# Optimization experiments

Measured on AMD Instinct MI355X. Metric: run time of the kernel, lower is better.

The kernel has to match this reference:

```python
import jax, jax.numpy as jnp
import numpy as np

BETA = 10.0


def _read_buffer(alpha, B, s_b, pop):
    # alpha: [b], B: [b,S,H], s_b: [b,S]. Closed form of the saturating
    # sequential read: cumsum after i steps = min(prefix_sum(s_b)_i, alpha),
    # so weight_i = min(P_i, alpha) - min(P_{i-1}, alpha).
    P = jnp.cumsum(s_b, axis=1)
    Pc = jnp.minimum(P, alpha[:, None])
    w = Pc - jnp.concatenate([jnp.zeros_like(Pc[:, :1]), Pc[:, :-1]], axis=1)
    vec = jnp.einsum('bs,bsh->bh', w, B)
    return vec, (s_b - w if pop else s_b)


def _read_stack(alpha, V, s, pop):
    # V: [M,b,H], s: [M,b]; smaller index = closer to stack top (unused slots
    # above the top have s==0 and contribute nothing).
    P = jnp.cumsum(s, axis=0)                 # [M,b]
    a = alpha[None, :]
    Pc1 = jnp.minimum(P, a)                   # saturate at alpha (first read)
    Pc2 = jnp.minimum(P, 1.0 + a)             # saturate at 1+alpha (both reads)
    z = jnp.zeros_like(P[:1])
    w1 = Pc1 - jnp.concatenate([z, Pc1[:-1]], axis=0)
    wt = Pc2 - jnp.concatenate([z, Pc2[:-1]], axis=0)
    w2 = wt - w1
    v1 = jnp.einsum('mb,mbh->bh', w1, V)
    v2 = jnp.einsum('mb,mbh->bh', w2, V)
    return v1, v2, (s - wt if pop else s)


def _forward(x, emb_table, lstm_wih, lstm_whh, lstm_bih, lstm_bhh,
             alpha_w, alpha_b, tree_left_w, tree_left_b, tree_right_w,
             tree_right_b, l0_w, l0_b, l1_w, l1_b, l2_w, l2_b):
    b, S = x.shape
    H = emb_table.shape[1]
    time = 2 * S
    M = 1 + 2 * time                          # max stack depth
    B = emb_table[x]                          # [b,S,H]
    s_b0 = (x > 0).astype(jnp.float32)
    V0 = jnp.zeros((M, b, H), jnp.float32)    # initial sentinel at M-1 (zeros)
    s0 = jnp.zeros((M, b), jnp.float32)
    h0 = jnp.zeros((b, H), jnp.float32)
    c0 = jnp.zeros((b, H), jnp.float32)
    ones_b = jnp.ones((b,), jnp.float32)

    def step(carry, t):
        s_b, V, s, h, c = carry
        n = 1 + 2 * t                         # current number of stack items
        x_b, _ = _read_buffer(ones_b, B, s_b, False)
        x1, x2, _ = _read_stack(ones_b, V, s, False)
        xt = jnp.concatenate([x_b, x1, x2], axis=1)
        # LSTMCell (torch gate order i,f,g,o)
        g = xt @ lstm_wih.T + lstm_bih + h @ lstm_whh.T + lstm_bhh
        gi, gf, gg, go = jnp.split(g, 4, axis=1)
        c = jax.nn.sigmoid(gf) * c + jax.nn.sigmoid(gi) * jnp.tanh(gg)
        h = jax.nn.sigmoid(go) * jnp.tanh(c)
        alphas = jax.nn.softmax(BETA * (h @ alpha_w.T + alpha_b), axis=1)
        a_r, a_s = alphas[:, 0], alphas[:, 1]
        # reduce: pop ~2 items, treeLSTM, push result with strength alpha_r
        r1, r2, s = _read_stack(a_r, V, s, True)
        tg = r1 @ tree_left_w.T + tree_left_b + r2 @ tree_right_w.T + tree_right_b
        ta, ti, tf1, tf2, to = jnp.split(tg, 5, axis=1)
        ct = jnp.tanh(ta) * jax.nn.sigmoid(ti) + jax.nn.sigmoid(tf1) * r1 + jax.nn.sigmoid(tf2) * r2
        ht = jax.nn.sigmoid(to) * jnp.tanh(ct)
        idx = M - (n + 1)
        V = V.at[idx].set(ht)
        s = s.at[idx].set(a_r)
        # shift: pop from buffer with strength alpha_s, push onto stack
        buf, s_b = _read_buffer(a_s, B, s_b, True)
        idx2 = M - (n + 2)
        V = V.at[idx2].set(buf)
        s = s.at[idx2].set(a_s)
        return (s_b, V, s, h, c), None

    carry, _ = jax.lax.scan(jax.checkpoint(step), (s_b0, V0, s0, h0, c0),
                            jnp.arange(time))
    s_b, V, s, h, c = carry
    x1, _, _ = _read_stack(ones_b, V, s, False)
    # MLP head
    y = jax.nn.relu(x1 @ l0_w.T + l0_b)
    y = jax.nn.relu(y @ l1_w.T + l1_b)
    return y @ l2_w.T + l2_b


def setup_inputs() -> dict:
    key = jax.random.key(0)
    ks = jax.random.split(key, 12)
    b, S, H, V, MLP, C = 64, 48, 256, 50257, 1024, 3
    sc = 0.05
    return {
        'x': jax.random.randint(ks[0], (b, S), 0, V, dtype=jnp.int32).astype(jnp.int64),
        'emb_table': jax.random.normal(ks[1], (V, H), jnp.float32) * sc,
        'lstm_wih': jax.random.normal(ks[2], (4 * H, 3 * H), jnp.float32) * sc,
        'lstm_whh': jax.random.normal(ks[3], (4 * H, H), jnp.float32) * sc,
        'lstm_bih': jnp.zeros((4 * H,), jnp.float32),
        'lstm_bhh': jnp.zeros((4 * H,), jnp.float32),
        'alpha_w': jax.random.normal(ks[4], (2, H), jnp.float32) * sc,
        'alpha_b': jnp.zeros((2,), jnp.float32),
        'tree_left_w': jax.random.normal(ks[5], (5 * H, H), jnp.float32) * sc,
        'tree_left_b': jnp.zeros((5 * H,), jnp.float32),
        'tree_right_w': jax.random.normal(ks[6], (5 * H, H), jnp.float32) * sc,
        'tree_right_b': jnp.zeros((5 * H,), jnp.float32),
        'l0_w': jax.random.normal(ks[7], (MLP, H), jnp.float32) * sc,
        'l0_b': jnp.zeros((MLP,), jnp.float32),
        'l1_w': jax.random.normal(ks[8], (MLP, MLP), jnp.float32) * sc,
        'l1_b': jnp.zeros((MLP,), jnp.float32),
        'l2_w': jax.random.normal(ks[9], (C, MLP), jnp.float32) * sc,
        'l2_b': jnp.zeros((C,), jnp.float32),
    }


def reference(x, emb_table, lstm_wih, lstm_whh, lstm_bih, lstm_bhh, alpha_w,
              alpha_b, tree_left_w, tree_left_b, tree_right_w, tree_right_b,
              l0_w, l0_b, l1_w, l1_b, l2_w, l2_b):
    return _forward(x, emb_table, lstm_wih, lstm_whh, lstm_bih, lstm_bhh,
                    alpha_w, alpha_b, tree_left_w, tree_left_b, tree_right_w,
                    tree_right_b, l0_w, l0_b, l1_w, l1_b, l2_w, l2_b)
```

## Files before the change

### kernel.cpp

```cpp
#include <hip/hip_runtime.h>
#include <math.h>

#define NBLK 1024
#define NTHR 256

typedef float vf4 __attribute__((ext_vector_type(4)));

namespace spinn {

constexpr int Ss = 48, Hh = 256, TT = 96, Mm = 193, H3 = 768, MLPD = 1024;

__device__ __forceinline__ float sigf(float x) { return 1.0f / (1.0f + expf(-x)); }

#define FMA4(acc, a, b)                         \
    {                                           \
        acc.x = fmaf((a).x, (b).x, acc.x);      \
        acc.y = fmaf((a).y, (b).y, acc.y);      \
        acc.z = fmaf((a).z, (b).z, acc.z);      \
        acc.w = fmaf((a).w, (b).w, acc.w);      \
    }

__device__ __forceinline__ void st_co(float* p, float v) {
    asm volatile("global_store_dword %0, %1, off sc0 sc1" :: "v"(p), "v"(v) : "memory");
}
__device__ __forceinline__ void ld_co_v4_1(const vf4* p0, vf4& r0) {
    asm volatile("global_load_dwordx4 %0, %1, off sc0 sc1\n\t"
                 "s_waitcnt vmcnt(0)"
                 : "=&v"(r0) : "v"(p0) : "memory");
}
__device__ __forceinline__ void ld_co_f1x4(const float* p0, const float* p1, const float* p2,
                                           const float* p3, float& r0, float& r1, float& r2, float& r3) {
    asm volatile("global_load_dword %0, %4, off sc0 sc1\n\t"
                 "global_load_dword %1, %5, off sc0 sc1\n\t"
                 "global_load_dword %2, %6, off sc0 sc1\n\t"
                 "global_load_dword %3, %7, off sc0 sc1\n\t"
                 "s_waitcnt vmcnt(0)"
                 : "=&v"(r0), "=&v"(r1), "=&v"(r2), "=&v"(r3)
                 : "v"(p0), "v"(p1), "v"(p2), "v"(p3) : "memory");
}
__device__ __forceinline__ unsigned ld_co_u32(const unsigned* p) {
    unsigned r;
    asm volatile("global_load_dword %0, %1, off sc0 sc1\n\t"
                 "s_waitcnt vmcnt(0)"
                 : "=&v"(r) : "v"(p) : "memory");
    return r;
}

__device__ __forceinline__ void gbar(unsigned* cnt, unsigned tgt) {
    asm volatile("s_waitcnt vmcnt(0)" ::: "memory");
    __syncthreads();
    if (threadIdx.x == 0) {
        unsigned one = 1u;
        asm volatile("global_atomic_add %0, %1, off" :: "v"(cnt), "v"(one) : "memory");
        while (ld_co_u32(cnt) < tgt) __builtin_amdgcn_s_sleep(1);
    }
    __syncthreads();
}

__device__ __forceinline__ float wave_iscan(float v, int lane) {
    #pragma unroll
    for (int off = 1; off < 64; off <<= 1) {
        float u = __shfl_up(v, off, 64);
        if (lane >= off) v += u;
    }
    return v;
}
__device__ __forceinline__ float wred64(float v) {
    #pragma unroll
    for (int off = 1; off < 64; off <<= 1) v += __shfl_xor(v, off, 64);
    return v;
}
__device__ __forceinline__ float wred_ms(float v) {
    v += __shfl_xor(v, 16, 64);
    v += __shfl_xor(v, 32, 64);
    return v;
}

}

using namespace spinn;

__global__ void __launch_bounds__(NTHR, 4) spinn_kernel(
    const int* __restrict__ x, const float* __restrict__ emb,
    const float* __restrict__ wih, const float* __restrict__ whh,
    const float* __restrict__ bih, const float* __restrict__ bhh,
    const float* __restrict__ aw, const float* __restrict__ ab,
    const float* __restrict__ tlw, const float* __restrict__ tlb,
    const float* __restrict__ trw, const float* __restrict__ trb,
    const float* __restrict__ l0w, const float* __restrict__ l0b,
    const float* __restrict__ l1w, const float* __restrict__ l1b,
    const float* __restrict__ l2w, const float* __restrict__ l2b,
    float* __restrict__ out, float* __restrict__ wsf, unsigned* __restrict__ bar)
{
    const int tid  = threadIdx.x;
    const int bid  = blockIdx.x;
    const int e    = bid >> 4;
    const int q    = bid & 15;
    const int db   = q * 16;
    const int wave = tid >> 6;
    const int lane = tid & 63;
    const int ms   = lane >> 4;
    const int dl   = lane & 15;

    unsigned* cnt = bar + e * 32;
    unsigned barnum = 0;

    float* XTg = wsf;
    float* Hbg = XTg + 64 * H3;
    float* R1g = Hbg + 64 * Hh;
    float* R2g = R1g + 64 * Hh;
    float* Y0g = R2g + 64 * Hh;
    float* Y1g = Y0g + 64 * MLPD;

    __shared__ float s_V[196 * 16];
    __shared__ float s_B[Ss * 16];
    __shared__ float s_xt[H3];
    __shared__ float s_h[256];
    __shared__ float s_c[16];
    __shared__ float s_g[64];
    __shared__ float s_tg[80];
    __shared__ float s_r1[256], s_r2[256];
    __shared__ float s_s[208];
    __shared__ float sw1[208], sw2[208];
    __shared__ float pw1[208], pw2[208];
    __shared__ float s_sb[Ss], s_wb[Ss], s_wbe[Ss];
    __shared__ float s_bias[64];
    __shared__ float s_tbias[80];

    float* s_y = s_V;

    {
        if (tid < 192) {
            int s = tid >> 2, j = tid & 3;
            int tok = x[e * Ss + s];
            ((vf4*)s_B)[tid] = ((const vf4*)emb)[(size_t)tok * 64 + q * 4 + j];
        }
        if (tid < Ss) s_sb[tid] = (x[e * Ss + tid] > 0) ? 1.0f : 0.0f;
        for (int i = tid; i < 208; i += NTHR) s_s[i] = 0.0f;
        if (tid < 256) s_h[tid] = 0.0f;
        if (tid < 16) s_c[tid] = 0.0f;
        if (tid < 64) {
            int row = (tid >> 4) * Hh + db + (tid & 15);
            s_bias[tid] = bih[row] + bhh[row];
        }
        if (tid < 80) {
            int row = (tid >> 4) * Hh + db + (tid & 15);
            s_tbias[tid] = tlb[row] + trb[row];
        }
        for (int i = tid; i < 196 * 16; i += NTHR) s_V[i] = 0.0f;
        __syncthreads();
        if (wave == 0) {
            float sbv = (lane < Ss) ? s_sb[lane] : 0.0f;
            float P = wave_iscan(sbv, lane);
            float wbe = fminf(P, 1.0f) - fminf(P - sbv, 1.0f);
            if (lane < Ss) s_wbe[lane] = wbe;
            float axb = 0.0f;
            #pragma unroll
            for (int j = 0; j < 12; j++) {
                int s = ms * 12 + j;
                axb = fmaf(s_wbe[s], s_B[s * 16 + dl], axb);
            }
            axb = wred_ms(axb);
            if (lane < 16) {
                float* xte = XTg + (size_t)e * H3;
                st_co(xte + db + dl, axb);
                st_co(xte + 256 + db + dl, 0.0f);
                st_co(xte + 512 + db + dl, 0.0f);
            }
        }
    }
    gbar(cnt, ++barnum * 16);

    for (int t = 0; t < TT; t++) {
        const int idx  = 191 - 2 * t;
        const int idx2 = idx - 1;

        {
            if (tid < 192) {
                vf4 v;
                ld_co_v4_1((const vf4*)XTg + (size_t)e * 192 + tid, v);
                ((vf4*)s_xt)[tid] = v;
            }
            __syncthreads();
            vf4 xr0 = ((const vf4*)s_xt)[lane];
            vf4 xr1 = ((const vf4*)s_xt)[64 + lane];
            vf4 xr2 = ((const vf4*)s_xt)[128 + lane];
            vf4 hr  = ((const vf4*)s_h)[lane];
            #pragma unroll 2
            for (int p = 0; p < 16; p++) {
                int r = wave * 16 + p;
                int row = (wave << 8) + db + p;
                const vf4* w  = (const vf4*)wih + (size_t)row * 192;
                const vf4* wh = (const vf4*)whh + (size_t)row * 64;
                vf4 w0 = w[lane], w1 = w[64 + lane], w2 = w[128 + lane], w3 = wh[lane];
                vf4 acc = {0.f, 0.f, 0.f, 0.f};
                FMA4(acc, w0, xr0); FMA4(acc, w1, xr1);
                FMA4(acc, w2, xr2); FMA4(acc, w3, hr);
                float sv = wred64(acc.x + acc.y + acc.z + acc.w);
                if (lane == 0) s_g[r] = sv + s_bias[r];
            }
            __syncthreads();
            if (tid < 16) {
                float gi = s_g[tid], gf = s_g[16 + tid], gg = s_g[32 + tid], go = s_g[48 + tid];
                float cv = sigf(gf) * s_c[tid] + sigf(gi) * tanhf(gg);
                s_c[tid] = cv;
                float hv = sigf(go) * tanhf(cv);
                st_co(Hbg + (size_t)e * Hh + db + tid, hv);
            }
        }
        gbar(cnt, ++barnum * 16);

        if (wave < 2) {
            float h0, h1, h2, h3;
            const float* hb = Hbg + (size_t)e * Hh + lane;
            ld_co_f1x4(hb, hb + 64, hb + 128, hb + 192, h0, h1, h2, h3);
            if (wave == 0) {
                s_h[lane] = h0;       s_h[64 + lane] = h1;
                s_h[128 + lane] = h2; s_h[192 + lane] = h3;
            }
            float lg0 = h0 * aw[lane] + h1 * aw[64 + lane] + h2 * aw[128 + lane] + h3 * aw[192 + lane];
            float lg1 = h0 * aw[256 + lane] + h1 * aw[320 + lane] + h2 * aw[384 + lane] + h3 * aw[448 + lane];
            lg0 = wred64(lg0) + ab[0];
            lg1 = wred64(lg1) + ab[1];
            float a_r = 1.0f / (1.0f + expf(10.0f * (lg1 - lg0)));
            float a_s = 1.0f / (1.0f + expf(10.0f * (lg0 - lg1)));

            if (wave == 0) {
                int m0 = lane * 4;
                float v0 = (m0     < Mm) ? s_s[m0]     : 0.0f;
                float v1 = (m0 + 1 < Mm) ? s_s[m0 + 1] : 0.0f;
                float v2 = (m0 + 2 < Mm) ? s_s[m0 + 2] : 0.0f;
                float v3 = (m0 + 3 < Mm) ? s_s[m0 + 3] : 0.0f;
                float c1 = v0 + v1, c2 = c1 + v2, c3 = c2 + v3;
                float inc = c3;
                #pragma unroll
                for (int off = 1; off < 64; off <<= 1) {
                    float u = __shfl_up(inc, off, 64);
                    if (lane >= off) inc += u;
                }
                float ex = inc - c3;
                float Pv[4]  = {ex + v0, ex + c1, ex + c2, ex + c3};
                float Pp[4]  = {ex, ex + v0, ex + c1, ex + c2};
                float vv_[4] = {v0, v1, v2, v3};
                float sn[4];
                #pragma unroll
                for (int i = 0; i < 4; i++) {
                    int m = m0 + i;
                    float w1 = fminf(Pv[i], a_r) - fminf(Pp[i], a_r);
                    float wt = fminf(Pv[i], 1.0f + a_r) - fminf(Pp[i], 1.0f + a_r);
                    float s2 = vv_[i] - wt;
                    if (m == idx)  s2 = a_r;
                    if (m == idx2) s2 = a_s;
                    sn[i] = s2;
                    if (m < Mm) {
                        sw1[m] = w1;
                        sw2[m] = wt - w1;
                        s_s[m] = s2;
                    } else if (m < 208) {
                        sw1[m] = 0.0f; sw2[m] = 0.0f;
                    }
                }
                float d1 = sn[0] + sn[1], d2 = d1 + sn[2], d3 = d2 + sn[3];
                float inc2 = d3;
                #pragma unroll
                for (int off = 1; off < 64; off <<= 1) {
                    float u = __shfl_up(inc2, off, 64);
                    if (lane >= off) inc2 += u;
                }
                float ex2 = inc2 - d3;
                float Qv[4] = {ex2 + sn[0], ex2 + d1, ex2 + d2, ex2 + d3};
                float Qp[4] = {ex2, ex2 + sn[0], ex2 + d1, ex2 + d2};
                #pragma unroll
                for (int i = 0; i < 4; i++) {
                    int m = m0 + i;
                    if (m < Mm) {
                        float w1e = fminf(Qv[i], 1.0f) - fminf(Qp[i], 1.0f);
                        pw1[m] = w1e;
                        pw2[m] = (fminf(Qv[i], 2.0f) - fminf(Qp[i], 2.0f)) - w1e;
                    } else if (m < 208) {
                        pw1[m] = 0.0f; pw2[m] = 0.0f;
                    }
                }
                float a1 = 0.0f, a2 = 0.0f;
                #pragma unroll 7
                for (int k = 0; k < 49; k++) {
                    int m = ms * 49 + k;
                    float vv = s_V[m * 16 + dl];
                    a1 = fmaf(sw1[m], vv, a1);
                    a2 = fmaf(sw2[m], vv, a2);
                }
                a1 = wred_ms(a1); a2 = wred_ms(a2);
                if (lane < 16) {
                    st_co(R1g + (size_t)e * Hh + db + dl, a1);
                    st_co(R2g + (size_t)e * Hh + db + dl, a2);
                }
            } else {
                float sbv = (lane < Ss) ? s_sb[lane] : 0.0f;
                float Pb = wave_iscan(sbv, lane);
                float wb = fminf(Pb, a_s) - fminf(Pb - sbv, a_s);
                float sbn = sbv - wb;
                float Pb2 = wave_iscan(sbn, lane);
                float wbe = fminf(Pb2, 1.0f) - fminf(Pb2 - sbn, 1.0f);
                if (lane < Ss) { s_sb[lane] = sbn; s_wb[lane] = wb; s_wbe[lane] = wbe; }
                float abf = 0.0f, axb = 0.0f;
                #pragma unroll
                for (int j = 0; j < 12; j++) {
                    int s = ms * 12 + j;
                    float be = s_B[s * 16 + dl];
                    abf = fmaf(s_wb[s], be, abf);
                    axb = fmaf(s_wbe[s], be, axb);
                }
                abf = wred_ms(abf); axb = wred_ms(axb);
                if (lane < 16) {
                    s_V[idx2 * 16 + dl] = abf;
                    st_co(XTg + (size_t)e * H3 + db + dl, axb);
                }
            }
        }
        gbar(cnt, ++barnum * 16);

        {
            if (tid < 64) {
                vf4 v; ld_co_v4_1((const vf4*)R1g + (size_t)e * 64 + tid, v);
                ((vf4*)s_r1)[tid] = v;
            } else if (tid < 128) {
                vf4 v; ld_co_v4_1((const vf4*)R2g + (size_t)e * 64 + (tid - 64), v);
                ((vf4*)s_r2)[tid - 64] = v;
            }
            __syncthreads();
            vf4 r1v = ((const vf4*)s_r1)[lane];
            vf4 r2v = ((const vf4*)s_r2)[lane];
            #pragma unroll 2
            for (int p = 0; p < 20; p++) {
                int r = wave * 20 + p;
                int row = ((r >> 4) << 8) + db + (r & 15);
                const vf4* wl = (const vf4*)tlw + (size_t)row * 64;
                const vf4* wr = (const vf4*)trw + (size_t)row * 64;
                vf4 u = wl[lane], v = wr[lane];
                vf4 acc = {0.f, 0.f, 0.f, 0.f};
                FMA4(acc, u, r1v); FMA4(acc, v, r2v);
                float sv = wred64(acc.x + acc.y + acc.z + acc.w);
                if (lane == 0) s_tg[r] = sv + s_tbias[r];
            }
            __syncthreads();
            if (tid < 16) {
                float ta  = s_tg[tid];
                float ti  = s_tg[16 + tid];
                float tf1 = s_tg[32 + tid];
                float tf2 = s_tg[48 + tid];
                float to  = s_tg[64 + tid];
                float r1d = s_r1[db + tid];
                float r2d = s_r2[db + tid];
                float ct = tanhf(ta) * sigf(ti) + sigf(tf1) * r1d + sigf(tf2) * r2d;
                s_V[idx * 16 + tid] = sigf(to) * tanhf(ct);
            }
            __syncthreads();
            if (wave == 0) {
                float x1 = 0.0f, x2 = 0.0f;
                #pragma unroll 7
                for (int k = 0; k < 49; k++) {
                    int m = ms * 49 + k;
                    float vv = s_V[m * 16 + dl];
                    x1 = fmaf(pw1[m], vv, x1);
                    x2 = fmaf(pw2[m], vv, x2);
                }
                x1 = wred_ms(x1); x2 = wred_ms(x2);
                if (lane < 16) {
                    st_co(XTg + (size_t)e * H3 + 256 + db + dl, x1);
                    st_co(XTg + (size_t)e * H3 + 512 + db + dl, x2);
                }
            }
        }
        gbar(cnt, ++barnum * 16);
    }

    {
        if (tid < 64) {
            vf4 v; ld_co_v4_1((const vf4*)XTg + (size_t)e * 192 + 64 + tid, v);
            ((vf4*)s_y)[tid] = v;
        }
        __syncthreads();
        vf4 xin = ((const vf4*)s_y)[lane];
        #pragma unroll 2
        for (int p = 0; p < 16; p++) {
            int row = q * 64 + wave * 16 + p;
            const vf4* w = (const vf4*)l0w + (size_t)row * 64;
            vf4 wv = w[lane];
            vf4 acc = {0.f, 0.f, 0.f, 0.f};
            FMA4(acc, wv, xin);
            float sv = wred64(acc.x + acc.y + acc.z + acc.w);
            if (lane == 0) st_co(Y0g + (size_t)e * MLPD + row, fmaxf(sv + l0b[row], 0.0f));
        }
    }
    gbar(cnt, ++barnum * 16);
    {
        {
            vf4 v; ld_co_v4_1((const vf4*)Y0g + (size_t)e * 256 + tid, v);
            ((vf4*)s_y)[tid] = v;
        }
        __syncthreads();
        vf4 y0 = ((const vf4*)s_y)[lane],       y1 = ((const vf4*)s_y)[64 + lane];
        vf4 y2 = ((const vf4*)s_y)[128 + lane], y3 = ((const vf4*)s_y)[192 + lane];
        #pragma unroll 2
        for (int p = 0; p < 16; p++) {
            int row = q * 64 + wave * 16 + p;
            const vf4* w = (const vf4*)l1w + (size_t)row * 256;
            vf4 w0 = w[lane], w1 = w[64 + lane], w2 = w[128 + lane], w3 = w[192 + lane];
            vf4 acc = {0.f, 0.f, 0.f, 0.f};
            FMA4(acc, w0, y0); FMA4(acc, w1, y1); FMA4(acc, w2, y2); FMA4(acc, w3, y3);
            float sv = wred64(acc.x + acc.y + acc.z + acc.w);
            if (lane == 0) st_co(Y1g + (size_t)e * MLPD + row, fmaxf(sv + l1b[row], 0.0f));
        }
    }
    gbar(cnt, ++barnum * 16);
    if (q == 0) {
        {
            vf4 v; ld_co_v4_1((const vf4*)Y1g + (size_t)e * 256 + tid, v);
            ((vf4*)s_y)[tid] = v;
        }
        __syncthreads();
        if (tid < 192) {
            int r = tid >> 6;
            const vf4* w = (const vf4*)l2w + (size_t)r * 256;
            vf4 acc = {0.f, 0.f, 0.f, 0.f};
            #pragma unroll
            for (int j = 0; j < 4; j++) {
                vf4 wv = w[lane + j * 64], yv = ((const vf4*)s_y)[lane + j * 64];
                FMA4(acc, wv, yv);
            }
            float sv = wred64(acc.x + acc.y + acc.z + acc.w);
            if (lane == 0) out[e * 3 + r] = sv + l2b[r];
        }
    }
}

extern "C" void kernel_launch(void* const* d_in, const int* in_sizes, int n_in,
                              void* d_out, int out_size, void* d_ws, size_t ws_size,
                              hipStream_t stream) {
    (void)in_sizes; (void)n_in; (void)out_size; (void)ws_size;
    (void)hipMemsetAsync(d_ws, 0, 8192, stream);

    const int*   x_   = (const int*)d_in[0];
    const float* emb  = (const float*)d_in[1];
    const float* wih  = (const float*)d_in[2];
    const float* whh  = (const float*)d_in[3];
    const float* bih  = (const float*)d_in[4];
    const float* bhh  = (const float*)d_in[5];
    const float* aw   = (const float*)d_in[6];
    const float* ab   = (const float*)d_in[7];
    const float* tlw  = (const float*)d_in[8];
    const float* tlb  = (const float*)d_in[9];
    const float* trw  = (const float*)d_in[10];
    const float* trb  = (const float*)d_in[11];
    const float* l0w  = (const float*)d_in[12];
    const float* l0b  = (const float*)d_in[13];
    const float* l1w  = (const float*)d_in[14];
    const float* l1b  = (const float*)d_in[15];
    const float* l2w  = (const float*)d_in[16];
    const float* l2b  = (const float*)d_in[17];

    float* wsf = (float*)((char*)d_ws + 8192);
    unsigned* bar = (unsigned*)d_ws;

    spinn_kernel<<<dim3(NBLK), dim3(NTHR), 0, stream>>>(
        x_, emb, wih, whh, bih, bhh, aw, ab, tlw, tlb, trw, trb,
        l0w, l0b, l1w, l1b, l2w, l2b, (float*)d_out, wsf, bar);
}
```

Baseline: 3.185 ms.

## Distribute alpha logits, precompute stack-read partials, and shorten the per-step critical path

Each block now computes its own partial of the alpha-gate logits right after the LSTM cell and publishes it to a small global array. The next phase reduces those 32 partials instead of every block reloading the full hidden state and doing a 256-wide dot. The x1/x2 stack reads are computed ahead of time by a spare wave, excluding the slot that has not been written yet. The final step then adds only the new slot's contribution, which removes a block barrier and a 49-step loop from the tree phase's serial tail. The hidden state is also loaded by otherwise idle threads during the LSTM phase, and several loop unroll factors are raised. The cost is an extra scratch buffer and more coherent global stores per step.

```diff
diff --git a/kernel.cpp b/kernel.cpp
--- a/kernel.cpp
+++ b/kernel.cpp
@@ -28,15 +28,12 @@
                  "s_waitcnt vmcnt(0)"
                  : "=&v"(r0) : "v"(p0) : "memory");
 }
-__device__ __forceinline__ void ld_co_f1x4(const float* p0, const float* p1, const float* p2,
-                                           const float* p3, float& r0, float& r1, float& r2, float& r3) {
-    asm volatile("global_load_dword %0, %4, off sc0 sc1\n\t"
-                 "global_load_dword %1, %5, off sc0 sc1\n\t"
-                 "global_load_dword %2, %6, off sc0 sc1\n\t"
-                 "global_load_dword %3, %7, off sc0 sc1\n\t"
+__device__ __forceinline__ float ld_co_f1(const float* p) {
+    float r;
+    asm volatile("global_load_dword %0, %1, off sc0 sc1\n\t"
                  "s_waitcnt vmcnt(0)"
-                 : "=&v"(r0), "=&v"(r1), "=&v"(r2), "=&v"(r3)
-                 : "v"(p0), "v"(p1), "v"(p2), "v"(p3) : "memory");
+                 : "=&v"(r) : "v"(p) : "memory");
+    return r;
 }
 __device__ __forceinline__ unsigned ld_co_u32(const unsigned* p) {
     unsigned r;
@@ -111,6 +108,7 @@
     float* R2g = R1g + 64 * Hh;
     float* Y0g = R2g + 64 * Hh;
     float* Y1g = Y0g + 64 * MLPD;
+    float* AP  = Y1g + 64 * MLPD;
 
     __shared__ float s_V[196 * 16];
     __shared__ float s_B[Ss * 16];
@@ -124,6 +122,8 @@
     __shared__ float sw1[208], sw2[208];
     __shared__ float pw1[208], pw2[208];
     __shared__ float s_sb[Ss], s_wb[Ss], s_wbe[Ss];
+    __shared__ float s_wx[2];
+    __shared__ float s_xp1[16], s_xp2[16];
     __shared__ float s_bias[64];
     __shared__ float s_tbias[80];
 
@@ -137,8 +137,10 @@
         }
         if (tid < Ss) s_sb[tid] = (x[e * Ss + tid] > 0) ? 1.0f : 0.0f;
         for (int i = tid; i < 208; i += NTHR) s_s[i] = 0.0f;
-        if (tid < 256) s_h[tid] = 0.0f;
-        if (tid < 16) s_c[tid] = 0.0f;
+        if (tid < 16) {
+            s_c[tid] = 0.0f;
+            st_co(Hbg + (size_t)e * Hh + db + tid, 0.0f);
+        }
         if (tid < 64) {
             int row = (tid >> 4) * Hh + db + (tid & 15);
             s_bias[tid] = bih[row] + bhh[row];
@@ -180,13 +182,17 @@
                 vf4 v;
                 ld_co_v4_1((const vf4*)XTg + (size_t)e * 192 + tid, v);
                 ((vf4*)s_xt)[tid] = v;
+            } else {
+                vf4 v;
+                ld_co_v4_1((const vf4*)Hbg + (size_t)e * 64 + (tid - 192), v);
+                ((vf4*)s_h)[tid - 192] = v;
             }
             __syncthreads();
             vf4 xr0 = ((const vf4*)s_xt)[lane];
             vf4 xr1 = ((const vf4*)s_xt)[64 + lane];
             vf4 xr2 = ((const vf4*)s_xt)[128 + lane];
             vf4 hr  = ((const vf4*)s_h)[lane];
-            #pragma unroll 2
+            #pragma unroll 4
             for (int p = 0; p < 16; p++) {
                 int r = wave * 16 + p;
                 int row = (wave << 8) + db + p;
@@ -206,25 +212,35 @@
                 s_c[tid] = cv;
                 float hv = sigf(go) * tanhf(cv);
                 st_co(Hbg + (size_t)e * Hh + db + tid, hv);
+                float p0 = hv * aw[db + tid];
+                float p1 = hv * aw[256 + db + tid];
+                #pragma unroll
+                for (int off = 1; off < 16; off <<= 1) {
+                    p0 += __shfl_xor(p0, off, 64);
+                    p1 += __shfl_xor(p1, off, 64);
+                }
+                if (tid == 0) {
+                    st_co(AP + e * 32 + q * 2, p0);
+                    st_co(AP + e * 32 + q * 2 + 1, p1);
+                }
             }
         }
         gbar(cnt, ++barnum * 16);
 
-        if (wave < 2) {
-            float h0, h1, h2, h3;
-            const float* hb = Hbg + (size_t)e * Hh + lane;
-            ld_co_f1x4(hb, hb + 64, hb + 128, hb + 192, h0, h1, h2, h3);
-            if (wave == 0) {
-                s_h[lane] = h0;       s_h[64 + lane] = h1;
-                s_h[128 + lane] = h2; s_h[192 + lane] = h3;
-            }
-            float lg0 = h0 * aw[lane] + h1 * aw[64 + lane] + h2 * aw[128 + lane] + h3 * aw[192 + lane];
-            float lg1 = h0 * aw[256 + lane] + h1 * aw[320 + lane] + h2 * aw[384 + lane] + h3 * aw[448 + lane];
-            lg0 = wred64(lg0) + ab[0];
-            lg1 = wred64(lg1) + ab[1];
-            float a_r = 1.0f / (1.0f + expf(10.0f * (lg1 - lg0)));
-            float a_s = 1.0f / (1.0f + expf(10.0f * (lg0 - lg1)));
-
+        {
+            float a_r = 0.0f, a_s = 0.0f;
+            if (wave < 2) {
+                float apv = 0.0f;
+                if (lane < 32) apv = ld_co_f1(AP + e * 32 + lane);
+                apv += __shfl_xor(apv, 2, 64);
+                apv += __shfl_xor(apv, 4, 64);
+                apv += __shfl_xor(apv, 8, 64);
+                apv += __shfl_xor(apv, 16, 64);
+                float lg0 = __shfl(apv, 0, 64) + ab[0];
+                float lg1 = __shfl(apv, 1, 64) + ab[1];
+                a_r = 1.0f / (1.0f + expf(10.0f * (lg1 - lg0)));
+                a_s = 1.0f / (1.0f + expf(10.0f * (lg0 - lg1)));
+            }
             if (wave == 0) {
                 int m0 = lane * 4;
                 float v0 = (m0     < Mm) ? s_s[m0]     : 0.0f;
@@ -275,26 +291,15 @@
                     int m = m0 + i;
                     if (m < Mm) {
                         float w1e = fminf(Qv[i], 1.0f) - fminf(Qp[i], 1.0f);
+                        float w2e = (fminf(Qv[i], 2.0f) - fminf(Qp[i], 2.0f)) - w1e;
                         pw1[m] = w1e;
-                        pw2[m] = (fminf(Qv[i], 2.0f) - fminf(Qp[i], 2.0f)) - w1e;
+                        pw2[m] = w2e;
+                        if (m == idx) { s_wx[0] = w1e; s_wx[1] = w2e; }
                     } else if (m < 208) {
                         pw1[m] = 0.0f; pw2[m] = 0.0f;
                     }
                 }
-                float a1 = 0.0f, a2 = 0.0f;
-                #pragma unroll 7
-                for (int k = 0; k < 49; k++) {
-                    int m = ms * 49 + k;
-                    float vv = s_V[m * 16 + dl];
-                    a1 = fmaf(sw1[m], vv, a1);
-                    a2 = fmaf(sw2[m], vv, a2);
-                }
-                a1 = wred_ms(a1); a2 = wred_ms(a2);
-                if (lane < 16) {
-                    st_co(R1g + (size_t)e * Hh + db + dl, a1);
-                    st_co(R2g + (size_t)e * Hh + db + dl, a2);
-                }
-            } else {
+            } else if (wave == 1) {
                 float sbv = (lane < Ss) ? s_sb[lane] : 0.0f;
                 float Pb = wave_iscan(sbv, lane);
                 float wb = fminf(Pb, a_s) - fminf(Pb - sbv, a_s);
@@ -316,6 +321,33 @@
                     st_co(XTg + (size_t)e * H3 + db + dl, axb);
                 }
             }
+            __syncthreads();
+            if (wave == 0) {
+                float a1 = 0.0f, a2 = 0.0f;
+                #pragma unroll 7
+                for (int k = 0; k < 49; k++) {
+                    int m = ms * 49 + k;
+                    float vv = s_V[m * 16 + dl];
+                    a1 = fmaf(sw1[m], vv, a1);
+                    a2 = fmaf(sw2[m], vv, a2);
+                }
+                a1 = wred_ms(a1); a2 = wred_ms(a2);
+                if (lane < 16) {
+                    st_co(R1g + (size_t)e * Hh + db + dl, a1);
+                    st_co(R2g + (size_t)e * Hh + db + dl, a2);
+                }
+            } else if (wave == 2) {
+                float x1 = 0.0f, x2 = 0.0f;
+                #pragma unroll 7
+                for (int k = 0; k < 49; k++) {
+                    int m = ms * 49 + k;
+                    float vv = s_V[m * 16 + dl];
+                    x1 = fmaf(pw1[m], vv, x1);
+                    x2 = fmaf(pw2[m], vv, x2);
+                }
+                x1 = wred_ms(x1); x2 = wred_ms(x2);
+                if (lane < 16) { s_xp1[dl] = x1; s_xp2[dl] = x2; }
+            }
         }
         gbar(cnt, ++barnum * 16);
 
@@ -330,7 +362,7 @@
             __syncthreads();
             vf4 r1v = ((const vf4*)s_r1)[lane];
             vf4 r2v = ((const vf4*)s_r2)[lane];
-            #pragma unroll 2
+            #pragma unroll 4
             for (int p = 0; p < 20; p++) {
                 int r = wave * 20 + p;
                 int row = ((r >> 4) << 8) + db + (r & 15);
@@ -352,23 +384,12 @@
                 float r1d = s_r1[db + tid];
                 float r2d = s_r2[db + tid];
                 float ct = tanhf(ta) * sigf(ti) + sigf(tf1) * r1d + sigf(tf2) * r2d;
-                s_V[idx * 16 + tid] = sigf(to) * tanhf(ct);
-            }
-            __syncthreads();
-            if (wave == 0) {
-                float x1 = 0.0f, x2 = 0.0f;
-                #pragma unroll 7
-                for (int k = 0; k < 49; k++) {
-                    int m = ms * 49 + k;
-                    float vv = s_V[m * 16 + dl];
-                    x1 = fmaf(pw1[m], vv, x1);
-                    x2 = fmaf(pw2[m], vv, x2);
-                }
-                x1 = wred_ms(x1); x2 = wred_ms(x2);
-                if (lane < 16) {
-                    st_co(XTg + (size_t)e * H3 + 256 + db + dl, x1);
-                    st_co(XTg + (size_t)e * H3 + 512 + db + dl, x2);
-                }
+                float ht = sigf(to) * tanhf(ct);
+                s_V[idx * 16 + tid] = ht;
+                float x1f = fmaf(s_wx[0], ht, s_xp1[tid]);
+                float x2f = fmaf(s_wx[1], ht, s_xp2[tid]);
+                st_co(XTg + (size_t)e * H3 + 256 + db + tid, x1f);
+                st_co(XTg + (size_t)e * H3 + 512 + db + tid, x2f);
             }
         }
         gbar(cnt, ++barnum * 16);
@@ -381,7 +402,7 @@
         }
         __syncthreads();
         vf4 xin = ((const vf4*)s_y)[lane];
-        #pragma unroll 2
+        #pragma unroll 4
         for (int p = 0; p < 16; p++) {
             int row = q * 64 + wave * 16 + p;
             const vf4* w = (const vf4*)l0w + (size_t)row * 64;
@@ -401,7 +422,7 @@
         __syncthreads();
         vf4 y0 = ((const vf4*)s_y)[lane],       y1 = ((const vf4*)s_y)[64 + lane];
         vf4 y2 = ((const vf4*)s_y)[128 + lane], y3 = ((const vf4*)s_y)[192 + lane];
-        #pragma unroll 2
+        #pragma unroll 4
         for (int p = 0; p < 16; p++) {
             int row = q * 64 + wave * 16 + p;
             const vf4* w = (const vf4*)l1w + (size_t)row * 256;
```

Result: slower. 3.528 ms (+10.8%).

## Process two batch elements per block to share weight loads across elements

Applied to the files above, without the earlier changes.

Each block now handles a pair of batch elements with 512 threads, halving the grid to 512 blocks and 32 barrier groups. Every weight row loaded for the LSTM gates, tree composition and MLP layers is applied to both elements' activations, so weight traffic per element is halved. The buffer and stack bookkeeping is also spread across more waves so it can run concurrently. In exchange, shared memory per block roughly doubles, occupancy drops to two blocks per CU, and each barrier-synchronised step has more work per block.

```diff
diff --git a/kernel.cpp b/kernel.cpp
--- a/kernel.cpp
+++ b/kernel.cpp
@@ -1,8 +1,8 @@
 #include <hip/hip_runtime.h>
 #include <math.h>
 
-#define NBLK 1024
-#define NTHR 256
+#define NBLK 512
+#define NTHR 512
 
 typedef float vf4 __attribute__((ext_vector_type(4)));
 
@@ -80,7 +80,7 @@
 
 using namespace spinn;
 
-__global__ void __launch_bounds__(NTHR, 4) spinn_kernel(
+__global__ void __launch_bounds__(NTHR, 2) spinn_kernel(
     const int* __restrict__ x, const float* __restrict__ emb,
     const float* __restrict__ wih, const float* __restrict__ whh,
     const float* __restrict__ bih, const float* __restrict__ bhh,
@@ -94,15 +94,16 @@
 {
     const int tid  = threadIdx.x;
     const int bid  = blockIdx.x;
-    const int e    = bid >> 4;
+    const int ep   = bid >> 4;
     const int q    = bid & 15;
     const int db   = q * 16;
+    const int e0   = ep * 2;
     const int wave = tid >> 6;
     const int lane = tid & 63;
     const int ms   = lane >> 4;
     const int dl   = lane & 15;
 
-    unsigned* cnt = bar + e * 32;
+    unsigned* cnt = bar + ep * 32;
     unsigned barnum = 0;
 
     float* XTg = wsf;
@@ -112,33 +113,37 @@
     float* Y0g = R2g + 64 * Hh;
     float* Y1g = Y0g + 64 * MLPD;
 
-    __shared__ float s_V[196 * 16];
-    __shared__ float s_B[Ss * 16];
-    __shared__ float s_xt[H3];
-    __shared__ float s_h[256];
-    __shared__ float s_c[16];
-    __shared__ float s_g[64];
-    __shared__ float s_tg[80];
-    __shared__ float s_r1[256], s_r2[256];
-    __shared__ float s_s[208];
-    __shared__ float sw1[208], sw2[208];
-    __shared__ float pw1[208], pw2[208];
-    __shared__ float s_sb[Ss], s_wb[Ss], s_wbe[Ss];
+    __shared__ float s_V[2 * 196 * 16];
+    __shared__ float s_B[2 * Ss * 16];
+    __shared__ float s_xt[2 * H3];
+    __shared__ float s_h[2 * 256];
+    __shared__ float s_c[32];
+    __shared__ float s_g[128];
+    __shared__ float s_tg[160];
+    __shared__ float s_r1[2 * 256], s_r2[2 * 256];
+    __shared__ float s_s[2 * 208];
+    __shared__ float sw1[2 * 208], sw2[2 * 208];
+    __shared__ float pw1[2 * 208], pw2[2 * 208];
+    __shared__ float s_sb[2 * Ss], s_wb[2 * Ss], s_wbe[2 * Ss];
     __shared__ float s_bias[64];
     __shared__ float s_tbias[80];
 
     float* s_y = s_V;
 
     {
-        if (tid < 192) {
-            int s = tid >> 2, j = tid & 3;
-            int tok = x[e * Ss + s];
-            ((vf4*)s_B)[tid] = ((const vf4*)emb)[(size_t)tok * 64 + q * 4 + j];
-        }
-        if (tid < Ss) s_sb[tid] = (x[e * Ss + tid] > 0) ? 1.0f : 0.0f;
-        for (int i = tid; i < 208; i += NTHR) s_s[i] = 0.0f;
-        if (tid < 256) s_h[tid] = 0.0f;
-        if (tid < 16) s_c[tid] = 0.0f;
+        if (tid < 384) {
+            int el = tid / 192, r = tid % 192;
+            int s = r >> 2, j = r & 3;
+            int tok = x[(e0 + el) * Ss + s];
+            ((vf4*)s_B)[el * 192 + s * 4 + j] = ((const vf4*)emb)[(size_t)tok * 64 + q * 4 + j];
+        }
+        if (tid < 2 * Ss) {
+            int el = tid / Ss, s = tid % Ss;
+            s_sb[tid] = (x[(e0 + el) * Ss + s] > 0) ? 1.0f : 0.0f;
+        }
+        for (int i = tid; i < 2 * 208; i += NTHR) s_s[i] = 0.0f;
+        for (int i = tid; i < 2 * 256; i += NTHR) s_h[i] = 0.0f;
+        if (tid < 32) s_c[tid] = 0.0f;
         if (tid < 64) {
             int row = (tid >> 4) * Hh + db + (tid & 15);
             s_bias[tid] = bih[row] + bhh[row];
@@ -147,22 +152,23 @@
             int row = (tid >> 4) * Hh + db + (tid & 15);
             s_tbias[tid] = tlb[row] + trb[row];
         }
-        for (int i = tid; i < 196 * 16; i += NTHR) s_V[i] = 0.0f;
+        for (int i = tid; i < 2 * 196 * 16; i += NTHR) s_V[i] = 0.0f;
         __syncthreads();
-        if (wave == 0) {
-            float sbv = (lane < Ss) ? s_sb[lane] : 0.0f;
+        if (wave < 2) {
+            int el = wave;
+            float sbv = (lane < Ss) ? s_sb[el * Ss + lane] : 0.0f;
             float P = wave_iscan(sbv, lane);
             float wbe = fminf(P, 1.0f) - fminf(P - sbv, 1.0f);
-            if (lane < Ss) s_wbe[lane] = wbe;
+            if (lane < Ss) s_wbe[el * Ss + lane] = wbe;
             float axb = 0.0f;
             #pragma unroll
             for (int j = 0; j < 12; j++) {
                 int s = ms * 12 + j;
-                axb = fmaf(s_wbe[s], s_B[s * 16 + dl], axb);
+                axb = fmaf(s_wbe[el * Ss + s], s_B[el * 768 + s * 16 + dl], axb);
             }
             axb = wred_ms(axb);
             if (lane < 16) {
-                float* xte = XTg + (size_t)e * H3;
+                float* xte = XTg + (size_t)(e0 + el) * H3;
                 st_co(xte + db + dl, axb);
                 st_co(xte + 256 + db + dl, 0.0f);
                 st_co(xte + 512 + db + dl, 0.0f);
@@ -176,193 +182,230 @@
         const int idx2 = idx - 1;
 
         {
-            if (tid < 192) {
+            if (tid < 384) {
+                int el = tid / 192, r = tid % 192;
                 vf4 v;
-                ld_co_v4_1((const vf4*)XTg + (size_t)e * 192 + tid, v);
-                ((vf4*)s_xt)[tid] = v;
+                ld_co_v4_1((const vf4*)XTg + (size_t)(e0 + el) * 192 + r, v);
+                ((vf4*)s_xt)[el * 192 + r] = v;
             }
             __syncthreads();
-            vf4 xr0 = ((const vf4*)s_xt)[lane];
-            vf4 xr1 = ((const vf4*)s_xt)[64 + lane];
-            vf4 xr2 = ((const vf4*)s_xt)[128 + lane];
-            vf4 hr  = ((const vf4*)s_h)[lane];
+            const vf4* sxt4 = (const vf4*)s_xt;
+            const vf4* sh4  = (const vf4*)s_h;
+            vf4 xa0 = sxt4[lane], xa1 = sxt4[64 + lane], xa2 = sxt4[128 + lane];
+            vf4 xb0 = sxt4[192 + lane], xb1 = sxt4[256 + lane], xb2 = sxt4[320 + lane];
+            vf4 ha = sh4[lane], hb = sh4[64 + lane];
             #pragma unroll 2
-            for (int p = 0; p < 16; p++) {
-                int r = wave * 16 + p;
-                int row = (wave << 8) + db + p;
+            for (int p = 0; p < 8; p++) {
+                int r = wave * 8 + p;
+                int row = ((r >> 4) << 8) + db + (r & 15);
                 const vf4* w  = (const vf4*)wih + (size_t)row * 192;
                 const vf4* wh = (const vf4*)whh + (size_t)row * 64;
                 vf4 w0 = w[lane], w1 = w[64 + lane], w2 = w[128 + lane], w3 = wh[lane];
-                vf4 acc = {0.f, 0.f, 0.f, 0.f};
-                FMA4(acc, w0, xr0); FMA4(acc, w1, xr1);
-                FMA4(acc, w2, xr2); FMA4(acc, w3, hr);
-                float sv = wred64(acc.x + acc.y + acc.z + acc.w);
-                if (lane == 0) s_g[r] = sv + s_bias[r];
+                vf4 aa = {0.f, 0.f, 0.f, 0.f}, ab_ = {0.f, 0.f, 0.f, 0.f};
+                FMA4(aa, w0, xa0); FMA4(aa, w1, xa1); FMA4(aa, w2, xa2); FMA4(aa, w3, ha);
+                FMA4(ab_, w0, xb0); FMA4(ab_, w1, xb1); FMA4(ab_, w2, xb2); FMA4(ab_, w3, hb);
+                float sa = wred64(aa.x + aa.y + aa.z + aa.w);
+                float sb = wred64(ab_.x + ab_.y + ab_.z + ab_.w);
+                if (lane == 0) {
+                    s_g[r] = sa + s_bias[r];
+                    s_g[64 + r] = sb + s_bias[r];
+                }
             }
             __syncthreads();
-            if (tid < 16) {
-                float gi = s_g[tid], gf = s_g[16 + tid], gg = s_g[32 + tid], go = s_g[48 + tid];
+            if (tid < 32) {
+                int el = tid >> 4, d = tid & 15;
+                int base = el * 64;
+                float gi = s_g[base + d], gf = s_g[base + 16 + d];
+                float gg = s_g[base + 32 + d], go = s_g[base + 48 + d];
                 float cv = sigf(gf) * s_c[tid] + sigf(gi) * tanhf(gg);
                 s_c[tid] = cv;
                 float hv = sigf(go) * tanhf(cv);
-                st_co(Hbg + (size_t)e * Hh + db + tid, hv);
+                st_co(Hbg + (size_t)(e0 + el) * Hh + db + d, hv);
             }
         }
         gbar(cnt, ++barnum * 16);
 
-        if (wave < 2) {
-            float h0, h1, h2, h3;
-            const float* hb = Hbg + (size_t)e * Hh + lane;
-            ld_co_f1x4(hb, hb + 64, hb + 128, hb + 192, h0, h1, h2, h3);
-            if (wave == 0) {
-                s_h[lane] = h0;       s_h[64 + lane] = h1;
-                s_h[128 + lane] = h2; s_h[192 + lane] = h3;
-            }
-            float lg0 = h0 * aw[lane] + h1 * aw[64 + lane] + h2 * aw[128 + lane] + h3 * aw[192 + lane];
-            float lg1 = h0 * aw[256 + lane] + h1 * aw[320 + lane] + h2 * aw[384 + lane] + h3 * aw[448 + lane];
-            lg0 = wred64(lg0) + ab[0];
-            lg1 = wred64(lg1) + ab[1];
-            float a_r = 1.0f / (1.0f + expf(10.0f * (lg1 - lg0)));
-            float a_s = 1.0f / (1.0f + expf(10.0f * (lg0 - lg1)));
-
-            if (wave == 0) {
-                int m0 = lane * 4;
-                float v0 = (m0     < Mm) ? s_s[m0]     : 0.0f;
-                float v1 = (m0 + 1 < Mm) ? s_s[m0 + 1] : 0.0f;
-                float v2 = (m0 + 2 < Mm) ? s_s[m0 + 2] : 0.0f;
-                float v3 = (m0 + 3 < Mm) ? s_s[m0 + 3] : 0.0f;
-                float c1 = v0 + v1, c2 = c1 + v2, c3 = c2 + v3;
-                float inc = c3;
-                #pragma unroll
-                for (int off = 1; off < 64; off <<= 1) {
-                    float u = __shfl_up(inc, off, 64);
-                    if (lane >= off) inc += u;
-                }
-                float ex = inc - c3;
-                float Pv[4]  = {ex + v0, ex + c1, ex + c2, ex + c3};
-                float Pp[4]  = {ex, ex + v0, ex + c1, ex + c2};
-                float vv_[4] = {v0, v1, v2, v3};
-                float sn[4];
-                #pragma unroll
-                for (int i = 0; i < 4; i++) {
-                    int m = m0 + i;
-                    float w1 = fminf(Pv[i], a_r) - fminf(Pp[i], a_r);
-                    float wt = fminf(Pv[i], 1.0f + a_r) - fminf(Pp[i], 1.0f + a_r);
-                    float s2 = vv_[i] - wt;
-                    if (m == idx)  s2 = a_r;
-                    if (m == idx2) s2 = a_s;
-                    sn[i] = s2;
-                    if (m < Mm) {
-                        sw1[m] = w1;
-                        sw2[m] = wt - w1;
-                        s_s[m] = s2;
-                    } else if (m < 208) {
-                        sw1[m] = 0.0f; sw2[m] = 0.0f;
-                    }
-                }
-                float d1 = sn[0] + sn[1], d2 = d1 + sn[2], d3 = d2 + sn[3];
-                float inc2 = d3;
-                #pragma unroll
-                for (int off = 1; off < 64; off <<= 1) {
-                    float u = __shfl_up(inc2, off, 64);
-                    if (lane >= off) inc2 += u;
-                }
-                float ex2 = inc2 - d3;
-                float Qv[4] = {ex2 + sn[0], ex2 + d1, ex2 + d2, ex2 + d3};
-                float Qp[4] = {ex2, ex2 + sn[0], ex2 + d1, ex2 + d2};
-                #pragma unroll
-                for (int i = 0; i < 4; i++) {
-                    int m = m0 + i;
-                    if (m < Mm) {
-                        float w1e = fminf(Qv[i], 1.0f) - fminf(Qp[i], 1.0f);
-                        pw1[m] = w1e;
-                        pw2[m] = (fminf(Qv[i], 2.0f) - fminf(Qp[i], 2.0f)) - w1e;
-                    } else if (m < 208) {
-                        pw1[m] = 0.0f; pw2[m] = 0.0f;
-                    }
-                }
+        {
+            if (wave < 4) {
+                int el = wave & 1;
+                int e = e0 + el;
+                float h0, h1, h2, h3;
+                const float* hb = Hbg + (size_t)e * Hh + lane;
+                ld_co_f1x4(hb, hb + 64, hb + 128, hb + 192, h0, h1, h2, h3);
+                if (wave < 2) {
+                    s_h[el * 256 + lane] = h0;       s_h[el * 256 + 64 + lane] = h1;
+                    s_h[el * 256 + 128 + lane] = h2; s_h[el * 256 + 192 + lane] = h3;
+                }
+                float lg0 = h0 * aw[lane] + h1 * aw[64 + lane] + h2 * aw[128 + lane] + h3 * aw[192 + lane];
+                float lg1 = h0 * aw[256 + lane] + h1 * aw[320 + lane] + h2 * aw[384 + lane] + h3 * aw[448 + lane];
+                lg0 = wred64(lg0) + ab[0];
+                lg1 = wred64(lg1) + ab[1];
+                float a_r = 1.0f / (1.0f + expf(10.0f * (lg1 - lg0)));
+                float a_s = 1.0f / (1.0f + expf(10.0f * (lg0 - lg1)));
+
+                if (wave < 2) {
+                    int m0 = lane * 4;
+                    int sb_ = el * 208;
+                    float v0 = (m0     < Mm) ? s_s[sb_ + m0]     : 0.0f;
+                    float v1 = (m0 + 1 < Mm) ? s_s[sb_ + m0 + 1] : 0.0f;
+                    float v2 = (m0 + 2 < Mm) ? s_s[sb_ + m0 + 2] : 0.0f;
+                    float v3 = (m0 + 3 < Mm) ? s_s[sb_ + m0 + 3] : 0.0f;
+                    float c1 = v0 + v1, c2 = c1 + v2, c3 = c2 + v3;
+                    float inc = c3;
+                    #pragma unroll
+                    for (int off = 1; off < 64; off <<= 1) {
+                        float u = __shfl_up(inc, off, 64);
+                        if (lane >= off) inc += u;
+                    }
+                    float ex = inc - c3;
+                    float Pv[4]  = {ex + v0, ex + c1, ex + c2, ex + c3};
+                    float Pp[4]  = {ex, ex + v0, ex + c1, ex + c2};
+                    float vv_[4] = {v0, v1, v2, v3};
+                    float sn[4];
+                    #pragma unroll
+                    for (int i = 0; i < 4; i++) {
+                        int m = m0 + i;
+                        float w1 = fminf(Pv[i], a_r) - fminf(Pp[i], a_r);
+                        float wt = fminf(Pv[i], 1.0f + a_r) - fminf(Pp[i], 1.0f + a_r);
+                        float s2 = vv_[i] - wt;
+                        if (m == idx)  s2 = a_r;
+                        if (m == idx2) s2 = a_s;
+                        sn[i] = s2;
+                        if (m < Mm) {
+                            sw1[sb_ + m] = w1;
+                            sw2[sb_ + m] = wt - w1;
+                            s_s[sb_ + m] = s2;
+                        } else if (m < 208) {
+                            sw1[sb_ + m] = 0.0f; sw2[sb_ + m] = 0.0f;
+                        }
+                    }
+                    float d1 = sn[0] + sn[1], d2 = d1 + sn[2], d3 = d2 + sn[3];
+                    float inc2 = d3;
+                    #pragma unroll
+                    for (int off = 1; off < 64; off <<= 1) {
+                        float u = __shfl_up(inc2, off, 64);
+                        if (lane >= off) inc2 += u;
+                    }
+                    float ex2 = inc2 - d3;
+                    float Qv[4] = {ex2 + sn[0], ex2 + d1, ex2 + d2, ex2 + d3};
+                    float Qp[4] = {ex2, ex2 + sn[0], ex2 + d1, ex2 + d2};
+                    #pragma unroll
+                    for (int i = 0; i < 4; i++) {
+                        int m = m0 + i;
+                        if (m < Mm) {
+                            float w1e = fminf(Qv[i], 1.0f) - fminf(Qp[i], 1.0f);
+                            pw1[sb_ + m] = w1e;
+                            pw2[sb_ + m] = (fminf(Qv[i], 2.0f) - fminf(Qp[i], 2.0f)) - w1e;
+                        } else if (m < 208) {
+                            pw1[sb_ + m] = 0.0f; pw2[sb_ + m] = 0.0f;
+                        }
+                    }
+                } else {
+                    float sbv = (lane < Ss) ? s_sb[el * Ss + lane] : 0.0f;
+                    float Pb = wave_iscan(sbv, lane);
+                    float wb = fminf(Pb, a_s) - fminf(Pb - sbv, a_s);
+                    float sbn = sbv - wb;
+                    float Pb2 = wave_iscan(sbn, lane);
+                    float wbe = fminf(Pb2, 1.0f) - fminf(Pb2 - sbn, 1.0f);
+                    if (lane < Ss) {
+                        s_sb[el * Ss + lane] = sbn;
+                        s_wb[el * Ss + lane] = wb;
+                        s_wbe[el * Ss + lane] = wbe;
+                    }
+                    float abf = 0.0f, axb = 0.0f;
+                    #pragma unroll
+                    for (int j = 0; j < 12; j++) {
+                        int s = ms * 12 + j;
+                        float be = s_B[el * 768 + s * 16 + dl];
+                        abf = fmaf(s_wb[el * Ss + s], be, abf);
+                        axb = fmaf(s_wbe[el * Ss + s], be, axb);
+                    }
+                    abf = wred_ms(abf); axb = wred_ms(axb);
+                    if (lane < 16) {
+                        s_V[el * 3136 + idx2 * 16 + dl] = abf;
+                        st_co(XTg + (size_t)e * H3 + db + dl, axb);
+                    }
+                }
+            }
+            __syncthreads();
+            if (wave < 2) {
+                int el = wave, e = e0 + el;
                 float a1 = 0.0f, a2 = 0.0f;
                 #pragma unroll 7
                 for (int k = 0; k < 49; k++) {
                     int m = ms * 49 + k;
-                    float vv = s_V[m * 16 + dl];
-                    a1 = fmaf(sw1[m], vv, a1);
-                    a2 = fmaf(sw2[m], vv, a2);
+                    float vv = s_V[el * 3136 + m * 16 + dl];
+                    a1 = fmaf(sw1[el * 208 + m], vv, a1);
+                    a2 = fmaf(sw2[el * 208 + m], vv, a2);
                 }
                 a1 = wred_ms(a1); a2 = wred_ms(a2);
                 if (lane < 16) {
                     st_co(R1g + (size_t)e * Hh + db + dl, a1);
                     st_co(R2g + (size_t)e * Hh + db + dl, a2);
                 }
-            } else {
-                float sbv = (lane < Ss) ? s_sb[lane] : 0.0f;
-                float Pb = wave_iscan(sbv, lane);
-                float wb = fminf(Pb, a_s) - fminf(Pb - sbv, a_s);
-                float sbn = sbv - wb;
-                float Pb2 = wave_iscan(sbn, lane);
-                float wbe = fminf(Pb2, 1.0f) - fminf(Pb2 - sbn, 1.0f);
-                if (lane < Ss) { s_sb[lane] = sbn; s_wb[lane] = wb; s_wbe[lane] = wbe; }
-                float abf = 0.0f, axb = 0.0f;
-                #pragma unroll
-                for (int j = 0; j < 12; j++) {
-                    int s = ms * 12 + j;
-                    float be = s_B[s * 16 + dl];
-                    abf = fmaf(s_wb[s], be, abf);
-                    axb = fmaf(s_wbe[s], be, axb);
-                }
-                abf = wred_ms(abf); axb = wred_ms(axb);
-                if (lane < 16) {
-                    s_V[idx2 * 16 + dl] = abf;
-                    st_co(XTg + (size_t)e * H3 + db + dl, axb);
-                }
             }
         }
         gbar(cnt, ++barnum * 16);
 
         {
-            if (tid < 64) {
-                vf4 v; ld_co_v4_1((const vf4*)R1g + (size_t)e * 64 + tid, v);
-                ((vf4*)s_r1)[tid] = v;
-            } else if (tid < 128) {
-                vf4 v; ld_co_v4_1((const vf4*)R2g + (size_t)e * 64 + (tid - 64), v);
-                ((vf4*)s_r2)[tid - 64] = v;
+            if (tid < 256) {
+                int part = tid >> 6, r = tid & 63;
+                int el = part >> 1;
+                vf4 v;
+                if (part & 1) {
+                    ld_co_v4_1((const vf4*)R2g + (size_t)(e0 + el) * 64 + r, v);
+                    ((vf4*)s_r2)[el * 64 + r] = v;
+                } else {
+                    ld_co_v4_1((const vf4*)R1g + (size_t)(e0 + el) * 64 + r, v);
+                    ((vf4*)s_r1)[el * 64 + r] = v;
+                }
             }
             __syncthreads();
-            vf4 r1v = ((const vf4*)s_r1)[lane];
-            vf4 r2v = ((const vf4*)s_r2)[lane];
+            const vf4* sr14 = (const vf4*)s_r1;
+            const vf4* sr24 = (const vf4*)s_r2;
+            vf4 r1a = sr14[lane], r2a = sr24[lane];
+            vf4 r1b = sr14[64 + lane], r2b = sr24[64 + lane];
             #pragma unroll 2
-            for (int p = 0; p < 20; p++) {
-                int r = wave * 20 + p;
+            for (int p = 0; p < 10; p++) {
+                int r = wave * 10 + p;
                 int row = ((r >> 4) << 8) + db + (r & 15);
                 const vf4* wl = (const vf4*)tlw + (size_t)row * 64;
                 const vf4* wr = (const vf4*)trw + (size_t)row * 64;
                 vf4 u = wl[lane], v = wr[lane];
-                vf4 acc = {0.f, 0.f, 0.f, 0.f};
-                FMA4(acc, u, r1v); FMA4(acc, v, r2v);
-                float sv = wred64(acc.x + acc.y + acc.z + acc.w);
-                if (lane == 0) s_tg[r] = sv + s_tbias[r];
+                vf4 aa = {0.f, 0.f, 0.f, 0.f}, ab_ = {0.f, 0.f, 0.f, 0.f};
+                FMA4(aa, u, r1a); FMA4(aa, v, r2a);
+                FMA4(ab_, u, r1b); FMA4(ab_, v, r2b);
+                float sa = wred64(aa.x + aa.y + aa.z + aa.w);
+                float sb = wred64(ab_.x + ab_.y + ab_.z + ab_.w);
+                if (lane == 0) {
+                    s_tg[r] = sa + s_tbias[r];
+                    s_tg[80 + r] = sb + s_tbias[r];
+                }
             }
             __syncthreads();
-            if (tid < 16) {
-                float ta  = s_tg[tid];
-                float ti  = s_tg[16 + tid];
-                float tf1 = s_tg[32 + tid];
-                float tf2 = s_tg[48 + tid];
-                float to  = s_tg[64 + tid];
-                float r1d = s_r1[db + tid];
-                float r2d = s_r2[db + tid];
+            if (tid < 32) {
+                int el = tid >> 4, d = tid & 15;
+                int base = el * 80;
+                float ta  = s_tg[base + d];
+                float ti  = s_tg[base + 16 + d];
+                float tf1 = s_tg[base + 32 + d];
+                float tf2 = s_tg[base + 48 + d];
+                float to  = s_tg[base + 64 + d];
+                float r1d = s_r1[el * 256 + db + d];
+                float r2d = s_r2[el * 256 + db + d];
                 float ct = tanhf(ta) * sigf(ti) + sigf(tf1) * r1d + sigf(tf2) * r2d;
-                s_V[idx * 16 + tid] = sigf(to) * tanhf(ct);
+                s_V[el * 3136 + idx * 16 + d] = sigf(to) * tanhf(ct);
             }
             __syncthreads();
-            if (wave == 0) {
+            if (wave < 2) {
+                int el = wave, e = e0 + el;
                 float x1 = 0.0f, x2 = 0.0f;
                 #pragma unroll 7
                 for (int k = 0; k < 49; k++) {
                     int m = ms * 49 + k;
-                    float vv = s_V[m * 16 + dl];
-                    x1 = fmaf(pw1[m], vv, x1);
-                    x2 = fmaf(pw2[m], vv, x2);
+                    float vv = s_V[el * 3136 + m * 16 + dl];
+                    x1 = fmaf(pw1[el * 208 + m], vv, x1);
+                    x2 = fmaf(pw2[el * 208 + m], vv, x2);
                 }
                 x1 = wred_ms(x1); x2 = wred_ms(x2);
                 if (lane < 16) {
@@ -375,47 +418,63 @@
     }
 
     {
-        if (tid < 64) {
-            vf4 v; ld_co_v4_1((const vf4*)XTg + (size_t)e * 192 + 64 + tid, v);
-            ((vf4*)s_y)[tid] = v;
+        if (tid < 128) {
+            int el = tid >> 6, r = tid & 63;
+            vf4 v;
+            ld_co_v4_1((const vf4*)XTg + (size_t)(e0 + el) * 192 + 64 + r, v);
+            ((vf4*)s_y)[el * 64 + r] = v;
         }
         __syncthreads();
-        vf4 xin = ((const vf4*)s_y)[lane];
+        vf4 xina = ((const vf4*)s_y)[lane];
+        vf4 xinb = ((const vf4*)s_y)[64 + lane];
         #pragma unroll 2
-        for (int p = 0; p < 16; p++) {
-            int row = q * 64 + wave * 16 + p;
-            const vf4* w = (const vf4*)l0w + (size_t)row * 64;
-            vf4 wv = w[lane];
-            vf4 acc = {0.f, 0.f, 0.f, 0.f};
-            FMA4(acc, wv, xin);
-            float sv = wred64(acc.x + acc.y + acc.z + acc.w);
-            if (lane == 0) st_co(Y0g + (size_t)e * MLPD + row, fmaxf(sv + l0b[row], 0.0f));
+        for (int p = 0; p < 8; p++) {
+            int row = q * 64 + wave * 8 + p;
+            vf4 wv = ((const vf4*)l0w)[(size_t)row * 64 + lane];
+            vf4 aa = {0.f, 0.f, 0.f, 0.f}, ab_ = {0.f, 0.f, 0.f, 0.f};
+            FMA4(aa, wv, xina); FMA4(ab_, wv, xinb);
+            float sa = wred64(aa.x + aa.y + aa.z + aa.w);
+            float sb = wred64(ab_.x + ab_.y + ab_.z + ab_.w);
+            if (lane == 0) {
+                st_co(Y0g + (size_t)e0 * MLPD + row, fmaxf(sa + l0b[row], 0.0f));
+                st_co(Y0g + (size_t)(e0 + 1) * MLPD + row, fmaxf(sb + l0b[row], 0.0f));
+            }
         }
     }
     gbar(cnt, ++barnum * 16);
     {
         {
-            vf4 v; ld_co_v4_1((const vf4*)Y0g + (size_t)e * 256 + tid, v);
-            ((vf4*)s_y)[tid] = v;
+            int el = tid >> 8, r = tid & 255;
+            vf4 v;
+            ld_co_v4_1((const vf4*)Y0g + (size_t)(e0 + el) * 256 + r, v);
+            ((vf4*)s_y)[el * 256 + r] = v;
         }
         __syncthreads();
-        vf4 y0 = ((const vf4*)s_y)[lane],       y1 = ((const vf4*)s_y)[64 + lane];
-        vf4 y2 = ((const vf4*)s_y)[128 + lane], y3 = ((const vf4*)s_y)[192 + lane];
+        const vf4* sy4 = (const vf4*)s_y;
+        vf4 ya0 = sy4[lane], ya1 = sy4[64 + lane], ya2 = sy4[128 + lane], ya3 = sy4[192 + lane];
+        vf4 yb0 = sy4[256 + lane], yb1 = sy4[320 + lane], yb2 = sy4[384 + lane], yb3 = sy4[448 + lane];
         #pragma unroll 2
-        for (int p = 0; p < 16; p++) {
-            int row = q * 64 + wave * 16 + p;
+        for (int p = 0; p < 8; p++) {
+            int row = q * 64 + wave * 8 + p;
             const vf4* w = (const vf4*)l1w + (size_t)row * 256;
             vf4 w0 = w[lane], w1 = w[64 + lane], w2 = w[128 + lane], w3 = w[192 + lane];
-            vf4 acc = {0.f, 0.f, 0.f, 0.f};
-            FMA4(acc, w0, y0); FMA4(acc, w1, y1); FMA4(acc, w2, y2); FMA4(acc, w3, y3);
-            float sv = wred64(acc.x + acc.y + acc.z + acc.w);
-            if (lane == 0) st_co(Y1g + (size_t)e * MLPD + row, fmaxf(sv + l1b[row], 0.0f));
+            vf4 aa = {0.f, 0.f, 0.f, 0.f}, ab_ = {0.f, 0.f, 0.f, 0.f};
+            FMA4(aa, w0, ya0); FMA4(aa, w1, ya1); FMA4(aa, w2, ya2); FMA4(aa, w3, ya3);
+            FMA4(ab_, w0, yb0); FMA4(ab_, w1, yb1); FMA4(ab_, w2, yb2); FMA4(ab_, w3, yb3);
+            float sa = wred64(aa.x + aa.y + aa.z + aa.w);
+            float sb = wred64(ab_.x + ab_.y + ab_.z + ab_.w);
+            if (lane == 0) {
+                st_co(Y1g + (size_t)e0 * MLPD + row, fmaxf(sa + l1b[row], 0.0f));
+                st_co(Y1g + (size_t)(e0 + 1) * MLPD + row, fmaxf(sb + l1b[row], 0.0f));
+            }
         }
     }
     gbar(cnt, ++barnum * 16);
-    if (q == 0) {
-        {
-            vf4 v; ld_co_v4_1((const vf4*)Y1g + (size_t)e * 256 + tid, v);
+    if (q < 2) {
+        int e = e0 + q;
+        if (tid < 256) {
+            vf4 v;
+            ld_co_v4_1((const vf4*)Y1g + (size_t)e * 256 + tid, v);
             ((vf4*)s_y)[tid] = v;
         }
         __syncthreads();
@@ -438,7 +497,7 @@
                               void* d_out, int out_size, void* d_ws, size_t ws_size,
                               hipStream_t stream) {
     (void)in_sizes; (void)n_in; (void)out_size; (void)ws_size;
-    (void)hipMemsetAsync(d_ws, 0, 8192, stream);
+    (void)hipMemsetAsync(d_ws, 0, 4096, stream);
 
     const int*   x_   = (const int*)d_in[0];
     const float* emb  = (const float*)d_in[1];
@@ -459,7 +518,7 @@
     const float* l2w  = (const float*)d_in[16];
     const float* l2b  = (const float*)d_in[17];
 
-    float* wsf = (float*)((char*)d_ws + 8192);
+    float* wsf = (float*)((char*)d_ws + 4096);
     unsigned* bar = (unsigned*)d_ws;
 
     spinn_kernel<<<dim3(NBLK), dim3(NTHR), 0, stream>>>(
```

New measurement: 3.500 ms. 9.9% more time.
